# Performance work log

Measured on AMD Instinct MI355X. Metric: run time of the kernel, lower is better.

The kernel has to match this reference:

```python
import jax, jax.numpy as jnp
import numpy as np

B, N, D_IN, H = 4, 4096, 3072, 64
ADJ_DENSITY = 0.01


def _layernorm(x, g, b, eps=1e-5):
    mu = jnp.mean(x, axis=-1, keepdims=True)
    var = jnp.var(x, axis=-1, keepdims=True)
    return (x - mu) * jax.lax.rsqrt(var + eps) * g + b


def _gat(x, W, adj, concat):
    # x: [B, N, H], W: [H, H], adj: [N, N]
    Wh = jnp.matmul(x, W)                                   # [B, N, H]
    scores = jnp.einsum('bnh,bmh->bnm', Wh, Wh) / np.sqrt(H)  # [B, N, N]
    scores = jnp.where(adj > 0, scores, jnp.float32(-1e9))
    attn = jax.nn.softmax(scores, axis=2)                   # dropout: eval no-op
    h_prime = jnp.matmul(attn, Wh)                          # [B, N, H]
    return jax.nn.elu(h_prime) if concat else h_prime


def setup_inputs() -> dict:
    key = jax.random.key(0)
    ks = jax.random.split(key, 18)
    adj = (jax.random.uniform(ks[0], (N, N)) < ADJ_DENSITY).astype(jnp.float32)
    adj = jnp.maximum(adj, jnp.eye(N, dtype=jnp.float32))   # self loops

    def xavier(k, shape, gain=1.0):
        bound = gain * np.sqrt(6.0 / (shape[0] + shape[1]))
        return jax.random.uniform(k, shape, jnp.float32, -bound, bound)

    return {
        'stim_features': jax.random.normal(ks[1], (B, D_IN), jnp.float32),
        'adj': adj,
        'W_enc1': xavier(ks[2], (D_IN, 2 * H)),
        'b_enc1': jnp.zeros((2 * H,), jnp.float32),
        'ln_g': jnp.ones((2 * H,), jnp.float32),
        'ln_b': jnp.zeros((2 * H,), jnp.float32),
        'W_enc2': xavier(ks[3], (2 * H, H)),
        'b_enc2': jnp.zeros((H,), jnp.float32),
        'voxel_emb': jax.random.normal(ks[4], (N, H), jnp.float32) * 0.01,
        'W_gat1': xavier(ks[5], (H, H), gain=1.414),
        'W_gat2': xavier(ks[6], (H, H), gain=1.414),
        'skip1_W': xavier(ks[7], (H, H)),
        'skip1_b': jnp.zeros((H,), jnp.float32),
        'skip2_W': xavier(ks[8], (H, H)),
        'skip2_b': jnp.zeros((H,), jnp.float32),
        'ro_W': xavier(ks[9], (H, 1)),
        'ro_b': jnp.zeros((1,), jnp.float32),
    }


def reference(stim_features, adj, W_enc1, b_enc1, ln_g, ln_b, W_enc2, b_enc2,
              voxel_emb, W_gat1, W_gat2, skip1_W, skip1_b, skip2_W, skip2_b,
              ro_W, ro_b):
    # stim encoder: Linear -> LayerNorm -> GELU -> (Dropout eval) -> Linear
    g = stim_features @ W_enc1 + b_enc1                     # [B, 2H]
    g = _layernorm(g, ln_g, ln_b)
    g = jax.nn.gelu(g, approximate=False)
    g = g @ W_enc2 + b_enc2                                 # [B, H]

    x = g[:, None, :] + voxel_emb[None, :, :]               # [B, N, H]

    x_res = x
    x = _gat(x, W_gat1, adj, concat=True)
    x = x + (x_res @ skip1_W + skip1_b)

    x_res = x
    x = _gat(x, W_gat2, adj, concat=False)
    x = x + (x_res @ skip2_W + skip2_b)

    pred = (x @ ro_W + ro_b)[..., 0]                        # [B, N]
    return pred
```

## Files before the change

### kernel.cpp

```cpp
#include <hip/hip_runtime.h>
#include <math.h>

#define NB 4
#define NV 4096
#define DIN 3072
#define HD 64
#define CAP 80

typedef unsigned short u16;
typedef unsigned int u32;
typedef _Float16 h2 __attribute__((ext_vector_type(2)));

__device__ __forceinline__ float fdot2u(u32 v, u32 q, float c) {
#if __has_builtin(__builtin_amdgcn_fdot2)
  return __builtin_amdgcn_fdot2(__builtin_bit_cast(h2, v), __builtin_bit_cast(h2, q), c, false);
#else
  h2 a = __builtin_bit_cast(h2, v), b = __builtin_bit_cast(h2, q);
  return c + (float)a[0] * (float)b[0] + (float)a[1] * (float)b[1];
#endif
}

__device__ __forceinline__ h2 shx(h2 v, int off) {
  return __builtin_bit_cast(h2, (u32)__shfl_xor((int)__builtin_bit_cast(u32, v), off, 64));
}

__global__ __launch_bounds__(256) void pre_kernel(
    const float* __restrict__ adj, int* __restrict__ cnt, int* __restrict__ cols,
    const float* __restrict__ stim, const float* __restrict__ W1, float* __restrict__ part) {
  int bid = blockIdx.x;
  int t = threadIdx.x;
  if (bid < NV) {
    int row = bid;
    int l = t & 63, w = t >> 6;
    __shared__ int wtot[4];
    __shared__ int stot;
    const float4* p = (const float4*)(adj + (size_t)row * NV);
    float4 v0 = p[t], v1 = p[t + 256], v2 = p[t + 512], v3 = p[t + 768];
    int c = (v0.x > 0.f) + (v0.y > 0.f) + (v0.z > 0.f) + (v0.w > 0.f) +
            (v1.x > 0.f) + (v1.y > 0.f) + (v1.z > 0.f) + (v1.w > 0.f) +
            (v2.x > 0.f) + (v2.y > 0.f) + (v2.z > 0.f) + (v2.w > 0.f) +
            (v3.x > 0.f) + (v3.y > 0.f) + (v3.z > 0.f) + (v3.w > 0.f);
    int val = c;
#pragma unroll
    for (int off = 1; off < 64; off <<= 1) {
      int tmp = __shfl_up(val, off, 64);
      if (l >= off) val += tmp;
    }
    if (l == 63) wtot[w] = val;
    __syncthreads();
    int base = 0;
    for (int i = 0; i < w; ++i) base += wtot[i];
    if (t == 255) {
      int s = base + val;
      s = s > CAP ? CAP : s;
      cnt[row] = s;
      stot = s;
    }
    int o = base + (val - c);
    int* cr = cols + row * CAP;
#define EMIT(vv, jj) if ((vv) > 0.f) { if (o < CAP) cr[o] = (jj); ++o; }
    int j0 = t * 4, j1 = (t + 256) * 4, j2 = (t + 512) * 4, j3 = (t + 768) * 4;
    EMIT(v0.x, j0) EMIT(v0.y, j0 + 1) EMIT(v0.z, j0 + 2) EMIT(v0.w, j0 + 3)
    EMIT(v1.x, j1) EMIT(v1.y, j1 + 1) EMIT(v1.z, j1 + 2) EMIT(v1.w, j1 + 3)
    EMIT(v2.x, j2) EMIT(v2.y, j2 + 1) EMIT(v2.z, j2 + 2) EMIT(v2.w, j2 + 3)
    EMIT(v3.x, j3) EMIT(v3.y, j3 + 1) EMIT(v3.z, j3 + 2) EMIT(v3.w, j3 + 3)
#undef EMIT
    __syncthreads();
    if (t < CAP && t >= stot) cr[t] = 0;
  } else {
    int e = bid - NV;
    int c = e % 24;
    int b = e / 24;
    int j = t & 127, h = t >> 7;
    int k0 = c * 128 + h * 64;
    float acc = 0.f;
#pragma unroll 8
    for (int k = 0; k < 64; ++k)
      acc += stim[b * DIN + k0 + k] * W1[(size_t)(k0 + k) * 128 + j];
    part[((b * 24 + c) * 2 + h) * 128 + j] = acc;
  }
}

__global__ __launch_bounds__(256) void whsk1_kernel(
    const float* __restrict__ part, const float* __restrict__ b1,
    const float* __restrict__ lng, const float* __restrict__ lnb,
    const float* __restrict__ W2, const float* __restrict__ b2,
    const float* __restrict__ emb, const float* __restrict__ Wg,
    const float* __restrict__ Sw, const float* __restrict__ Sb,
    u16* __restrict__ Whh, float* __restrict__ Sk) {
  __shared__ float wgt[4096];
  __shared__ float swt[4096];
  __shared__ float xst[64 * 33];
  __shared__ float sbs[64];
  __shared__ float act[128];
  __shared__ float red[128];
  __shared__ __align__(16) float gs[64];
  __shared__ float s_mu, s_var;
  int tid = threadIdx.x;
  int base = blockIdx.x * 32;
  int b = base >> 12;

  for (int i = tid; i < 1024; i += 256) {
    ((float4*)wgt)[i] = ((const float4*)Wg)[i];
    ((float4*)swt)[i] = ((const float4*)Sw)[i];
  }
  if (tid < 64) sbs[tid] = Sb[tid];
  if (tid < 128) {
    float hv = 0.f;
    for (int c = 0; c < 48; ++c) hv += part[(b * 48 + c) * 128 + tid];
    hv += b1[tid];
    act[tid] = hv;
    red[tid] = hv;
  }
  __syncthreads();
  for (int s = 64; s > 0; s >>= 1) {
    if (tid < s) red[tid] += red[tid + s];
    __syncthreads();
  }
  if (tid == 0) s_mu = red[0] * (1.f / 128.f);
  __syncthreads();
  if (tid < 128) { float dv = act[tid] - s_mu; red[tid] = dv * dv; }
  __syncthreads();
  for (int s = 64; s > 0; s >>= 1) {
    if (tid < s) red[tid] += red[tid + s];
    __syncthreads();
  }
  if (tid == 0) s_var = red[0] * (1.f / 128.f);
  __syncthreads();
  if (tid < 128) {
    float y = (act[tid] - s_mu) * rsqrtf(s_var + 1e-5f) * lng[tid] + lnb[tid];
    act[tid] = 0.5f * y * (1.f + erff(y * 0.70710678118f));
  }
  __syncthreads();
  if (tid < 64) {
    float a2 = 0.f;
    for (int k = 0; k < 128; ++k) a2 += act[k] * W2[k * 64 + tid];
    gs[tid] = a2 + b2[tid];
  }
  __syncthreads();
  for (int i4 = tid; i4 < 512; i4 += 256) {
    int rr = i4 >> 4, k0 = (i4 & 15) * 4;
    int n = (base + rr) & (NV - 1);
    float4 gv = *(const float4*)(gs + k0);
    float4 ev = *(const float4*)(emb + (size_t)n * 64 + k0);
    xst[(k0 + 0) * 33 + rr] = gv.x + ev.x;
    xst[(k0 + 1) * 33 + rr] = gv.y + ev.y;
    xst[(k0 + 2) * 33 + rr] = gv.z + ev.z;
    xst[(k0 + 3) * 33 + rr] = gv.w + ev.w;
  }
  __syncthreads();
  int cg = tid & 15;
  int r0 = tid >> 4;
  float4 aw0 = make_float4(0, 0, 0, 0), as0 = make_float4(0, 0, 0, 0);
  float4 aw1 = make_float4(0, 0, 0, 0), as1 = make_float4(0, 0, 0, 0);
#pragma unroll 4
  for (int k = 0; k < 64; ++k) {
    float4 wv = *(const float4*)&wgt[k * 64 + 4 * cg];
    float4 sv = *(const float4*)&swt[k * 64 + 4 * cg];
    float x0 = xst[k * 33 + r0];
    float x1v = xst[k * 33 + r0 + 16];
    aw0.x = fmaf(x0, wv.x, aw0.x); aw0.y = fmaf(x0, wv.y, aw0.y);
    aw0.z = fmaf(x0, wv.z, aw0.z); aw0.w = fmaf(x0, wv.w, aw0.w);
    as0.x = fmaf(x0, sv.x, as0.x); as0.y = fmaf(x0, sv.y, as0.y);
    as0.z = fmaf(x0, sv.z, as0.z); as0.w = fmaf(x0, sv.w, as0.w);
    aw1.x = fmaf(x1v, wv.x, aw1.x); aw1.y = fmaf(x1v, wv.y, aw1.y);
    aw1.z = fmaf(x1v, wv.z, aw1.z); aw1.w = fmaf(x1v, wv.w, aw1.w);
    as1.x = fmaf(x1v, sv.x, as1.x); as1.y = fmaf(x1v, sv.y, as1.y);
    as1.z = fmaf(x1v, sv.z, as1.z); as1.w = fmaf(x1v, sv.w, as1.w);
  }
  float4 sb4 = *(const float4*)&sbs[4 * cg];
  int grow0 = base + r0, grow1 = base + r0 + 16;
  ushort4 h0, h1;
  h0.x = __builtin_bit_cast(u16, (_Float16)aw0.x);
  h0.y = __builtin_bit_cast(u16, (_Float16)aw0.y);
  h0.z = __builtin_bit_cast(u16, (_Float16)aw0.z);
  h0.w = __builtin_bit_cast(u16, (_Float16)aw0.w);
  h1.x = __builtin_bit_cast(u16, (_Float16)aw1.x);
  h1.y = __builtin_bit_cast(u16, (_Float16)aw1.y);
  h1.z = __builtin_bit_cast(u16, (_Float16)aw1.z);
  h1.w = __builtin_bit_cast(u16, (_Float16)aw1.w);
  *(ushort4*)(Whh + (size_t)grow0 * 64 + 4 * cg) = h0;
  *(ushort4*)(Whh + (size_t)grow1 * 64 + 4 * cg) = h1;
  *(float4*)(Sk + (size_t)grow0 * 64 + 4 * cg) =
      make_float4(as0.x + sb4.x, as0.y + sb4.y, as0.z + sb4.z, as0.w + sb4.w);
  *(float4*)(Sk + (size_t)grow1 * 64 + 4 * cg) =
      make_float4(as1.x + sb4.x, as1.y + sb4.y, as1.z + sb4.z, as1.w + sb4.w);
}

__global__ __launch_bounds__(512) void attn_l1_kernel(
    const u16* __restrict__ Whh, const float* __restrict__ Sk,
    const int* __restrict__ cnt, const int* __restrict__ cols,
    const float* __restrict__ Wg2, const float* __restrict__ Sw2, const float* __restrict__ Sb2,
    u16* __restrict__ Whh2, float* __restrict__ Sk2) {
  __shared__ float wgt[4096];
  __shared__ float swt[4096];
  __shared__ float sbs[64];
  __shared__ float xl[8][64];
  int tid = threadIdx.x;
  int lane = tid & 63;
  int w = tid >> 6;
  int bid = blockIdx.x;
  int x = bid & 7;
  int gidx = bid >> 3;
  int b = x >> 1;
  int rowhalf = x & 1;
  int n = __builtin_amdgcn_readfirstlane(rowhalf * 2048 + gidx * 8 + w);
  int wid = b * NV + n;
  const u16* whhbase = Whh + (size_t)b * (NV * HD);
  int nn = __builtin_amdgcn_readfirstlane(cnt[n]);
  const int* cl = cols + n * CAP;
  int q = lane & 3;
  int gq = lane >> 2;

  for (int i = tid; i < 1024; i += 512) {
    ((float4*)wgt)[i] = ((const float4*)Wg2)[i];
    ((float4*)swt)[i] = ((const float4*)Sw2)[i];
  }
  if (tid < 64) sbs[tid] = Sb2[tid];

  const uint4* qr = (const uint4*)(whhbase + (size_t)n * HD);
  uint4 QA = qr[q];
  uint4 QB = qr[q + 4];

  float s[5], p[5];
  uint4 SA0, SB0, SA1, SB1, SA2, SB2;
#define SCORE_BLOCK(jb, SAv, SBv)                                                                \
  {                                                                                              \
    int j = (jb) * 16 + gq;                                                                      \
    int m = cl[j];                                                                               \
    const uint4* vr = (const uint4*)(whhbase + (size_t)m * HD);                                  \
    SAv = vr[q];                                                                                 \
    SBv = vr[q + 4];                                                                             \
    float t = 0.f;                                                                               \
    t = fdot2u(SAv.x, QA.x, t);                                                                  \
    t = fdot2u(SAv.y, QA.y, t);                                                                  \
    t = fdot2u(SAv.z, QA.z, t);                                                                  \
    t = fdot2u(SAv.w, QA.w, t);                                                                  \
    t = fdot2u(SBv.x, QB.x, t);                                                                  \
    t = fdot2u(SBv.y, QB.y, t);                                                                  \
    t = fdot2u(SBv.z, QB.z, t);                                                                  \
    t = fdot2u(SBv.w, QB.w, t);                                                                  \
    t += __shfl_xor(t, 1, 64);                                                                   \
    t += __shfl_xor(t, 2, 64);                                                                   \
    s[jb] = (j < nn) ? t * 0.125f : -1e30f;                                                      \
  }
  SCORE_BLOCK(0, SA0, SB0)
  SCORE_BLOCK(1, SA1, SB1)
  SCORE_BLOCK(2, SA2, SB2)
  s[3] = -1e30f;
  s[4] = -1e30f;
  bool tail = (nn > 48);
  if (tail) {
    uint4 TA, TB;
    SCORE_BLOCK(3, TA, TB)
    SCORE_BLOCK(4, TA, TB)
  }
#undef SCORE_BLOCK

  float mx = fmaxf(fmaxf(fmaxf(s[0], s[1]), fmaxf(s[2], s[3])), s[4]);
  mx = fmaxf(mx, __shfl_xor(mx, 4, 64));
  mx = fmaxf(mx, __shfl_xor(mx, 8, 64));
  mx = fmaxf(mx, __shfl_xor(mx, 16, 64));
  mx = fmaxf(mx, __shfl_xor(mx, 32, 64));
  float sum = 0.f;
#pragma unroll
  for (int jb = 0; jb < 5; ++jb) {
    p[jb] = (jb * 16 + gq < nn) ? __expf(s[jb] - mx) : 0.f;
    sum += p[jb];
  }
  sum += __shfl_xor(sum, 4, 64);
  sum += __shfl_xor(sum, 8, 64);
  sum += __shfl_xor(sum, 16, 64);
  sum += __shfl_xor(sum, 32, 64);
  float inv = 1.f / sum;

  h2 aa[8];
#pragma unroll
  for (int k = 0; k < 8; ++k) aa[k] = h2{(_Float16)0, (_Float16)0};
#define PV_ACC(pp, Av, Bv)                                                                       \
  {                                                                                              \
    _Float16 pf = (_Float16)(pp);                                                                \
    h2 ph = {pf, pf};                                                                            \
    aa[0] += __builtin_bit_cast(h2, (Av).x) * ph;                                                \
    aa[1] += __builtin_bit_cast(h2, (Av).y) * ph;                                                \
    aa[2] += __builtin_bit_cast(h2, (Av).z) * ph;                                                \
    aa[3] += __builtin_bit_cast(h2, (Av).w) * ph;                                                \
    aa[4] += __builtin_bit_cast(h2, (Bv).x) * ph;                                                \
    aa[5] += __builtin_bit_cast(h2, (Bv).y) * ph;                                                \
    aa[6] += __builtin_bit_cast(h2, (Bv).z) * ph;                                                \
    aa[7] += __builtin_bit_cast(h2, (Bv).w) * ph;                                                \
  }
  PV_ACC(p[0], SA0, SB0)
  PV_ACC(p[1], SA1, SB1)
  PV_ACC(p[2], SA2, SB2)
  if (tail) {
    int m3 = cl[48 + gq];
    const uint4* vr3 = (const uint4*)(whhbase + (size_t)m3 * HD);
    uint4 A3 = vr3[q], B3 = vr3[q + 4];
    PV_ACC(p[3], A3, B3)
    if (nn > 64) {
      int m4 = cl[64 + gq];
      const uint4* vr4 = (const uint4*)(whhbase + (size_t)m4 * HD);
      uint4 A4 = vr4[q], B4 = vr4[q + 4];
      PV_ACC(p[4], A4, B4)
    }
  }
#undef PV_ACC

  bool g1 = (gq & 1) != 0;
  h2 bb[4];
#pragma unroll
  for (int i = 0; i < 4; ++i) {
    h2 k = g1 ? aa[i + 4] : aa[i];
    h2 u = g1 ? aa[i] : aa[i + 4];
    bb[i] = k + shx(u, 4);
  }
  bool g2 = (gq & 2) != 0;
  h2 cc[2];
#pragma unroll
  for (int i = 0; i < 2; ++i) {
    h2 k = g2 ? bb[i + 2] : bb[i];
    h2 u = g2 ? bb[i] : bb[i + 2];
    cc[i] = k + shx(u, 8);
  }
  bool g4 = (gq & 4) != 0;
  h2 dd;
  {
    h2 k = g4 ? cc[1] : cc[0];
    h2 u = g4 ? cc[0] : cc[1];
    dd = k + shx(u, 16);
  }
  dd = dd + shx(dd, 32);
  int a = 8 * q + 32 * (gq & 1) + 4 * ((gq >> 1) & 1) + 2 * ((gq >> 2) & 1);
  float f0 = (float)dd[0] * inv;
  float f1 = (float)dd[1] * inv;

  float2 sk2 = *(const float2*)(Sk + (size_t)wid * HD + a);
  float o0 = (f0 > 0.f ? f0 : (__expf(f0) - 1.f)) + sk2.x;
  float o1 = (f1 > 0.f ? f1 : (__expf(f1) - 1.f)) + sk2.y;
  if ((gq & 8) == 0) {
    xl[w][a] = o0;
    xl[w][a + 1] = o1;
  }
  __syncthreads();

  if (tid < 128) {
    int cg = tid & 15;
    int r = tid >> 4;
    float4 aw = make_float4(0, 0, 0, 0), as = make_float4(0, 0, 0, 0);
#pragma unroll 4
    for (int k = 0; k < 64; ++k) {
      float4 wv = *(const float4*)&wgt[k * 64 + 4 * cg];
      float4 sv = *(const float4*)&swt[k * 64 + 4 * cg];
      float xv = xl[r][k];
      aw.x = fmaf(xv, wv.x, aw.x); aw.y = fmaf(xv, wv.y, aw.y);
      aw.z = fmaf(xv, wv.z, aw.z); aw.w = fmaf(xv, wv.w, aw.w);
      as.x = fmaf(xv, sv.x, as.x); as.y = fmaf(xv, sv.y, as.y);
      as.z = fmaf(xv, sv.z, as.z); as.w = fmaf(xv, sv.w, as.w);
    }
    int n_r = rowhalf * 2048 + gidx * 8 + r;
    size_t wid_r = (size_t)(b * NV + n_r) * 64 + 4 * cg;
    float4 sb4 = *(const float4*)&sbs[4 * cg];
    ushort4 hh;
    hh.x = __builtin_bit_cast(u16, (_Float16)aw.x);
    hh.y = __builtin_bit_cast(u16, (_Float16)aw.y);
    hh.z = __builtin_bit_cast(u16, (_Float16)aw.z);
    hh.w = __builtin_bit_cast(u16, (_Float16)aw.w);
    *(ushort4*)(Whh2 + wid_r) = hh;
    *(float4*)(Sk2 + wid_r) =
        make_float4(as.x + sb4.x, as.y + sb4.y, as.z + sb4.z, as.w + sb4.w);
  }
}

__global__ __launch_bounds__(256) void attn_l2_kernel(
    const u16* __restrict__ Whh, const float* __restrict__ Sk,
    const int* __restrict__ cnt, const int* __restrict__ cols,
    const float* __restrict__ roW, const float* __restrict__ rob, float* __restrict__ out) {
  int tid = threadIdx.x;
  int lane = tid & 63;
  int w = tid >> 6;
  int bid = blockIdx.x;
  int x = bid & 7;
  int gidx = bid >> 3;
  int b = x >> 1;
  int n = __builtin_amdgcn_readfirstlane((x & 1) * 2048 + gidx * 4 + w);
  int wid = b * NV + n;
  const u16* whhbase = Whh + (size_t)b * (NV * HD);
  int nn = __builtin_amdgcn_readfirstlane(cnt[n]);
  const int* cl = cols + n * CAP;
  int q = lane & 3;
  int gq = lane >> 2;

  const uint4* qr = (const uint4*)(whhbase + (size_t)n * HD);
  uint4 QA = qr[q];
  uint4 QB = qr[q + 4];

  float s[5], p[5];
  uint4 SA0, SB0, SA1, SB1, SA2, SB2;
#define SCORE_BLOCK(jb, SAv, SBv)                                                                \
  {                                                                                              \
    int j = (jb) * 16 + gq;                                                                      \
    int m = cl[j];                                                                               \
    const uint4* vr = (const uint4*)(whhbase + (size_t)m * HD);                                  \
    SAv = vr[q];                                                                                 \
    SBv = vr[q + 4];                                                                             \
    float t = 0.f;                                                                               \
    t = fdot2u(SAv.x, QA.x, t);                                                                  \
    t = fdot2u(SAv.y, QA.y, t);                                                                  \
    t = fdot2u(SAv.z, QA.z, t);                                                                  \
    t = fdot2u(SAv.w, QA.w, t);                                                                  \
    t = fdot2u(SBv.x, QB.x, t);                                                                  \
    t = fdot2u(SBv.y, QB.y, t);                                                                  \
    t = fdot2u(SBv.z, QB.z, t);                                                                  \
    t = fdot2u(SBv.w, QB.w, t);                                                                  \
    t += __shfl_xor(t, 1, 64);                                                                   \
    t += __shfl_xor(t, 2, 64);                                                                   \
    s[jb] = (j < nn) ? t * 0.125f : -1e30f;                                                      \
  }
  SCORE_BLOCK(0, SA0, SB0)
  SCORE_BLOCK(1, SA1, SB1)
  SCORE_BLOCK(2, SA2, SB2)
  s[3] = -1e30f;
  s[4] = -1e30f;
  bool tail = (nn > 48);
  if (tail) {
    uint4 TA, TB;
    SCORE_BLOCK(3, TA, TB)
    SCORE_BLOCK(4, TA, TB)
  }
#undef SCORE_BLOCK

  float mx = fmaxf(fmaxf(fmaxf(s[0], s[1]), fmaxf(s[2], s[3])), s[4]);
  mx = fmaxf(mx, __shfl_xor(mx, 4, 64));
  mx = fmaxf(mx, __shfl_xor(mx, 8, 64));
  mx = fmaxf(mx, __shfl_xor(mx, 16, 64));
  mx = fmaxf(mx, __shfl_xor(mx, 32, 64));
  float sum = 0.f;
#pragma unroll
  for (int jb = 0; jb < 5; ++jb) {
    p[jb] = (jb * 16 + gq < nn) ? __expf(s[jb] - mx) : 0.f;
    sum += p[jb];
  }
  sum += __shfl_xor(sum, 4, 64);
  sum += __shfl_xor(sum, 8, 64);
  sum += __shfl_xor(sum, 16, 64);
  sum += __shfl_xor(sum, 32, 64);
  float inv = 1.f / sum;

  h2 aa[8];
#pragma unroll
  for (int k = 0; k < 8; ++k) aa[k] = h2{(_Float16)0, (_Float16)0};
#define PV_ACC(pp, Av, Bv)                                                                       \
  {                                                                                              \
    _Float16 pf = (_Float16)(pp);                                                                \
    h2 ph = {pf, pf};                                                                            \
    aa[0] += __builtin_bit_cast(h2, (Av).x) * ph;                                                \
    aa[1] += __builtin_bit_cast(h2, (Av).y) * ph;                                                \
    aa[2] += __builtin_bit_cast(h2, (Av).z) * ph;                                                \
    aa[3] += __builtin_bit_cast(h2, (Av).w) * ph;                                                \
    aa[4] += __builtin_bit_cast(h2, (Bv).x) * ph;                                                \
    aa[5] += __builtin_bit_cast(h2, (Bv).y) * ph;                                                \
    aa[6] += __builtin_bit_cast(h2, (Bv).z) * ph;                                                \
    aa[7] += __builtin_bit_cast(h2, (Bv).w) * ph;                                                \
  }
  PV_ACC(p[0], SA0, SB0)
  PV_ACC(p[1], SA1, SB1)
  PV_ACC(p[2], SA2, SB2)
  if (tail) {
    int m3 = cl[48 + gq];
    const uint4* vr3 = (const uint4*)(whhbase + (size_t)m3 * HD);
    uint4 A3 = vr3[q], B3 = vr3[q + 4];
    PV_ACC(p[3], A3, B3)
    if (nn > 64) {
      int m4 = cl[64 + gq];
      const uint4* vr4 = (const uint4*)(whhbase + (size_t)m4 * HD);
      uint4 A4 = vr4[q], B4 = vr4[q + 4];
      PV_ACC(p[4], A4, B4)
    }
  }
#undef PV_ACC

  bool g1 = (gq & 1) != 0;
  h2 bb[4];
#pragma unroll
  for (int i = 0; i < 4; ++i) {
    h2 k = g1 ? aa[i + 4] : aa[i];
    h2 u = g1 ? aa[i] : aa[i + 4];
    bb[i] = k + shx(u, 4);
  }
  bool g2 = (gq & 2) != 0;
  h2 cc[2];
#pragma unroll
  for (int i = 0; i < 2; ++i) {
    h2 k = g2 ? bb[i + 2] : bb[i];
    h2 u = g2 ? bb[i] : bb[i + 2];
    cc[i] = k + shx(u, 8);
  }
  bool g4 = (gq & 4) != 0;
  h2 dd;
  {
    h2 k = g4 ? cc[1] : cc[0];
    h2 u = g4 ? cc[0] : cc[1];
    dd = k + shx(u, 16);
  }
  dd = dd + shx(dd, 32);
  int a = 8 * q + 32 * (gq & 1) + 4 * ((gq >> 1) & 1) + 2 * ((gq >> 2) & 1);
  float f0 = (float)dd[0] * inv;
  float f1 = (float)dd[1] * inv;

  float2 sk2 = *(const float2*)(Sk + (size_t)wid * HD + a);
  float2 ro2 = *(const float2*)(roW + a);
  float wsp = (f0 + sk2.x) * ro2.x + (f1 + sk2.y) * ro2.y;
  wsp += __shfl_xor(wsp, 1, 64);
  wsp += __shfl_xor(wsp, 2, 64);
  wsp += __shfl_xor(wsp, 4, 64);
  wsp += __shfl_xor(wsp, 8, 64);
  wsp += __shfl_xor(wsp, 16, 64);
  if (lane == 0) out[wid] = wsp + rob[0];
}

extern "C" void kernel_launch(void* const* d_in, const int* in_sizes, int n_in,
                              void* d_out, int out_size, void* d_ws, size_t ws_size,
                              hipStream_t stream) {
  const float* stim = (const float*)d_in[0];
  const float* adj  = (const float*)d_in[1];
  const float* W1   = (const float*)d_in[2];
  const float* b1   = (const float*)d_in[3];
  const float* lng  = (const float*)d_in[4];
  const float* lnb  = (const float*)d_in[5];
  const float* W2   = (const float*)d_in[6];
  const float* b2   = (const float*)d_in[7];
  const float* emb  = (const float*)d_in[8];
  const float* Wg1  = (const float*)d_in[9];
  const float* Wg2  = (const float*)d_in[10];
  const float* s1w  = (const float*)d_in[11];
  const float* s1b  = (const float*)d_in[12];
  const float* s2w  = (const float*)d_in[13];
  const float* s2b  = (const float*)d_in[14];
  const float* roW  = (const float*)d_in[15];
  const float* rob  = (const float*)d_in[16];
  float* out = (float*)d_out;

  char* ws = (char*)d_ws;
  float* part = (float*)(ws + 4096);
  int*   cnt  = (int*)(ws + 131072);
  int*   cols = (int*)(ws + 147456);
  u16*   Whh2 = (u16*)(ws + 1572864);
  float* Sk   = (float*)(ws + 5767168);
  float* Sk2  = (float*)(ws + 9961472);
  u16*   Whh  = (u16*)(ws + 14155776);

  pre_kernel<<<dim3(NV + 96), dim3(256), 0, stream>>>(adj, cnt, cols, stim, W1, part);
  whsk1_kernel<<<dim3(NB * NV / 32), dim3(256), 0, stream>>>(part, b1, lng, lnb, W2, b2,
                                                             emb, Wg1, s1w, s1b, Whh, Sk);
  attn_l1_kernel<<<dim3(NB * NV / 8), dim3(512), 0, stream>>>(Whh, Sk, cnt, cols,
                                                              Wg2, s2w, s2b, Whh2, Sk2);
  attn_l2_kernel<<<dim3(NB * NV / 4), dim3(256), 0, stream>>>(Whh2, Sk2, cnt, cols,
                                                              roW, rob, out);
}
```

Baseline: 61.13 us.

## Overlap adjacency compaction with Wh/skip projection by regrouping kernels

The encoder partial GEMV moves into its own small kernel. Adjacency CSR compaction and the Wh/skip1 projection are merged into one launch, so the large adjacency scan runs alongside the projection blocks instead of before them. The softmax exp for the tail neighbor blocks now runs only when the row has more than 48 neighbors. The merged kernel uses a union shared-memory buffer sized for the projection path, which may lower occupancy for the adjacency blocks.

```diff
diff --git a/kernel.cpp b/kernel.cpp
--- a/kernel.cpp
+++ b/kernel.cpp
@@ -24,16 +24,37 @@
   return __builtin_bit_cast(h2, (u32)__shfl_xor((int)__builtin_bit_cast(u32, v), off, 64));
 }
 
-__global__ __launch_bounds__(256) void pre_kernel(
+__global__ __launch_bounds__(256) void enc_a_kernel(const float* __restrict__ stim,
+                                                    const float* __restrict__ W1,
+                                                    float* __restrict__ part) {
+  int c = blockIdx.x;
+  int b = blockIdx.y;
+  int t = threadIdx.x;
+  int j = t & 127, h = t >> 7;
+  int k0 = c * 128 + h * 64;
+  float acc = 0.f;
+#pragma unroll 8
+  for (int k = 0; k < 64; ++k)
+    acc += stim[b * DIN + k0 + k] * W1[(size_t)(k0 + k) * 128 + j];
+  part[((b * 24 + c) * 2 + h) * 128 + j] = acc;
+}
+
+__global__ __launch_bounds__(256) void mid_kernel(
     const float* __restrict__ adj, int* __restrict__ cnt, int* __restrict__ cols,
-    const float* __restrict__ stim, const float* __restrict__ W1, float* __restrict__ part) {
+    const float* __restrict__ part, const float* __restrict__ b1,
+    const float* __restrict__ lng, const float* __restrict__ lnb,
+    const float* __restrict__ W2, const float* __restrict__ b2,
+    const float* __restrict__ emb, const float* __restrict__ Wg,
+    const float* __restrict__ Sw, const float* __restrict__ Sb,
+    u16* __restrict__ Whh, float* __restrict__ Sk) {
+  __shared__ __align__(16) char smem[42784];
   int bid = blockIdx.x;
   int t = threadIdx.x;
   if (bid < NV) {
+    int* wtot = (int*)smem;
+    int* stot = (int*)(smem + 16);
     int row = bid;
     int l = t & 63, w = t >> 6;
-    __shared__ int wtot[4];
-    __shared__ int stot;
     const float4* p = (const float4*)(adj + (size_t)row * NV);
     float4 v0 = p[t], v1 = p[t + 256], v2 = p[t + 512], v3 = p[t + 768];
     int c = (v0.x > 0.f) + (v0.y > 0.f) + (v0.z > 0.f) + (v0.w > 0.f) +
@@ -54,7 +75,7 @@
       int s = base + val;
       s = s > CAP ? CAP : s;
       cnt[row] = s;
-      stot = s;
+      *stot = s;
     }
     int o = base + (val - c);
     int* cr = cols + row * CAP;
@@ -66,125 +87,107 @@
     EMIT(v3.x, j3) EMIT(v3.y, j3 + 1) EMIT(v3.z, j3 + 2) EMIT(v3.w, j3 + 3)
 #undef EMIT
     __syncthreads();
-    if (t < CAP && t >= stot) cr[t] = 0;
+    if (t < CAP && t >= *stot) cr[t] = 0;
   } else {
-    int e = bid - NV;
-    int c = e % 24;
-    int b = e / 24;
-    int j = t & 127, h = t >> 7;
-    int k0 = c * 128 + h * 64;
-    float acc = 0.f;
-#pragma unroll 8
-    for (int k = 0; k < 64; ++k)
-      acc += stim[b * DIN + k0 + k] * W1[(size_t)(k0 + k) * 128 + j];
-    part[((b * 24 + c) * 2 + h) * 128 + j] = acc;
-  }
-}
-
-__global__ __launch_bounds__(256) void whsk1_kernel(
-    const float* __restrict__ part, const float* __restrict__ b1,
-    const float* __restrict__ lng, const float* __restrict__ lnb,
-    const float* __restrict__ W2, const float* __restrict__ b2,
-    const float* __restrict__ emb, const float* __restrict__ Wg,
-    const float* __restrict__ Sw, const float* __restrict__ Sb,
-    u16* __restrict__ Whh, float* __restrict__ Sk) {
-  __shared__ float wgt[4096];
-  __shared__ float swt[4096];
-  __shared__ float xst[64 * 33];
-  __shared__ float sbs[64];
-  __shared__ float act[128];
-  __shared__ float red[128];
-  __shared__ __align__(16) float gs[64];
-  __shared__ float s_mu, s_var;
-  int tid = threadIdx.x;
-  int base = blockIdx.x * 32;
-  int b = base >> 12;
-
-  for (int i = tid; i < 1024; i += 256) {
-    ((float4*)wgt)[i] = ((const float4*)Wg)[i];
-    ((float4*)swt)[i] = ((const float4*)Sw)[i];
-  }
-  if (tid < 64) sbs[tid] = Sb[tid];
-  if (tid < 128) {
-    float hv = 0.f;
-    for (int c = 0; c < 48; ++c) hv += part[(b * 48 + c) * 128 + tid];
-    hv += b1[tid];
-    act[tid] = hv;
-    red[tid] = hv;
-  }
-  __syncthreads();
-  for (int s = 64; s > 0; s >>= 1) {
-    if (tid < s) red[tid] += red[tid + s];
-    __syncthreads();
-  }
-  if (tid == 0) s_mu = red[0] * (1.f / 128.f);
-  __syncthreads();
-  if (tid < 128) { float dv = act[tid] - s_mu; red[tid] = dv * dv; }
-  __syncthreads();
-  for (int s = 64; s > 0; s >>= 1) {
-    if (tid < s) red[tid] += red[tid + s];
-    __syncthreads();
-  }
-  if (tid == 0) s_var = red[0] * (1.f / 128.f);
-  __syncthreads();
-  if (tid < 128) {
-    float y = (act[tid] - s_mu) * rsqrtf(s_var + 1e-5f) * lng[tid] + lnb[tid];
-    act[tid] = 0.5f * y * (1.f + erff(y * 0.70710678118f));
-  }
-  __syncthreads();
-  if (tid < 64) {
-    float a2 = 0.f;
-    for (int k = 0; k < 128; ++k) a2 += act[k] * W2[k * 64 + tid];
-    gs[tid] = a2 + b2[tid];
-  }
-  __syncthreads();
-  for (int i4 = tid; i4 < 512; i4 += 256) {
-    int rr = i4 >> 4, k0 = (i4 & 15) * 4;
-    int n = (base + rr) & (NV - 1);
-    float4 gv = *(const float4*)(gs + k0);
-    float4 ev = *(const float4*)(emb + (size_t)n * 64 + k0);
-    xst[(k0 + 0) * 33 + rr] = gv.x + ev.x;
-    xst[(k0 + 1) * 33 + rr] = gv.y + ev.y;
-    xst[(k0 + 2) * 33 + rr] = gv.z + ev.z;
-    xst[(k0 + 3) * 33 + rr] = gv.w + ev.w;
-  }
-  __syncthreads();
-  int cg = tid & 15;
-  int r0 = tid >> 4;
-  float4 aw0 = make_float4(0, 0, 0, 0), as0 = make_float4(0, 0, 0, 0);
-  float4 aw1 = make_float4(0, 0, 0, 0), as1 = make_float4(0, 0, 0, 0);
+    float* wgt = (float*)smem;
+    float* swt = (float*)(smem + 16384);
+    float* xst = (float*)(smem + 32768);
+    float* sbs = (float*)(smem + 41216);
+    float* act = (float*)(smem + 41472);
+    float* red = (float*)(smem + 41984);
+    float* gs  = (float*)(smem + 42496);
+    float* s_mu = (float*)(smem + 42752);
+    float* s_var = (float*)(smem + 42756);
+    int tid = t;
+    int base = (bid - NV) * 32;
+    int b = base >> 12;
+
+    for (int i = tid; i < 1024; i += 256) {
+      ((float4*)wgt)[i] = ((const float4*)Wg)[i];
+      ((float4*)swt)[i] = ((const float4*)Sw)[i];
+    }
+    if (tid < 64) sbs[tid] = Sb[tid];
+    if (tid < 128) {
+      float hv = 0.f;
+      for (int c = 0; c < 48; ++c) hv += part[(b * 48 + c) * 128 + tid];
+      hv += b1[tid];
+      act[tid] = hv;
+      red[tid] = hv;
+    }
+    __syncthreads();
+    for (int s = 64; s > 0; s >>= 1) {
+      if (tid < s) red[tid] += red[tid + s];
+      __syncthreads();
+    }
+    if (tid == 0) *s_mu = red[0] * (1.f / 128.f);
+    __syncthreads();
+    if (tid < 128) { float dv = act[tid] - *s_mu; red[tid] = dv * dv; }
+    __syncthreads();
+    for (int s = 64; s > 0; s >>= 1) {
+      if (tid < s) red[tid] += red[tid + s];
+      __syncthreads();
+    }
+    if (tid == 0) *s_var = red[0] * (1.f / 128.f);
+    __syncthreads();
+    if (tid < 128) {
+      float y = (act[tid] - *s_mu) * rsqrtf(*s_var + 1e-5f) * lng[tid] + lnb[tid];
+      act[tid] = 0.5f * y * (1.f + erff(y * 0.70710678118f));
+    }
+    __syncthreads();
+    if (tid < 64) {
+      float a2 = 0.f;
+      for (int k = 0; k < 128; ++k) a2 += act[k] * W2[k * 64 + tid];
+      gs[tid] = a2 + b2[tid];
+    }
+    __syncthreads();
+    for (int i4 = tid; i4 < 512; i4 += 256) {
+      int rr = i4 >> 4, k0 = (i4 & 15) * 4;
+      int n = (base + rr) & (NV - 1);
+      float4 gv = *(const float4*)(gs + k0);
+      float4 ev = *(const float4*)(emb + (size_t)n * 64 + k0);
+      xst[(k0 + 0) * 33 + rr] = gv.x + ev.x;
+      xst[(k0 + 1) * 33 + rr] = gv.y + ev.y;
+      xst[(k0 + 2) * 33 + rr] = gv.z + ev.z;
+      xst[(k0 + 3) * 33 + rr] = gv.w + ev.w;
+    }
+    __syncthreads();
+    int cg = tid & 15;
+    int r0 = tid >> 4;
+    float4 aw0 = make_float4(0, 0, 0, 0), as0 = make_float4(0, 0, 0, 0);
+    float4 aw1 = make_float4(0, 0, 0, 0), as1 = make_float4(0, 0, 0, 0);
 #pragma unroll 4
-  for (int k = 0; k < 64; ++k) {
-    float4 wv = *(const float4*)&wgt[k * 64 + 4 * cg];
-    float4 sv = *(const float4*)&swt[k * 64 + 4 * cg];
-    float x0 = xst[k * 33 + r0];
-    float x1v = xst[k * 33 + r0 + 16];
-    aw0.x = fmaf(x0, wv.x, aw0.x); aw0.y = fmaf(x0, wv.y, aw0.y);
-    aw0.z = fmaf(x0, wv.z, aw0.z); aw0.w = fmaf(x0, wv.w, aw0.w);
-    as0.x = fmaf(x0, sv.x, as0.x); as0.y = fmaf(x0, sv.y, as0.y);
-    as0.z = fmaf(x0, sv.z, as0.z); as0.w = fmaf(x0, sv.w, as0.w);
-    aw1.x = fmaf(x1v, wv.x, aw1.x); aw1.y = fmaf(x1v, wv.y, aw1.y);
-    aw1.z = fmaf(x1v, wv.z, aw1.z); aw1.w = fmaf(x1v, wv.w, aw1.w);
-    as1.x = fmaf(x1v, sv.x, as1.x); as1.y = fmaf(x1v, sv.y, as1.y);
-    as1.z = fmaf(x1v, sv.z, as1.z); as1.w = fmaf(x1v, sv.w, as1.w);
-  }
-  float4 sb4 = *(const float4*)&sbs[4 * cg];
-  int grow0 = base + r0, grow1 = base + r0 + 16;
-  ushort4 h0, h1;
-  h0.x = __builtin_bit_cast(u16, (_Float16)aw0.x);
-  h0.y = __builtin_bit_cast(u16, (_Float16)aw0.y);
-  h0.z = __builtin_bit_cast(u16, (_Float16)aw0.z);
-  h0.w = __builtin_bit_cast(u16, (_Float16)aw0.w);
-  h1.x = __builtin_bit_cast(u16, (_Float16)aw1.x);
-  h1.y = __builtin_bit_cast(u16, (_Float16)aw1.y);
-  h1.z = __builtin_bit_cast(u16, (_Float16)aw1.z);
-  h1.w = __builtin_bit_cast(u16, (_Float16)aw1.w);
-  *(ushort4*)(Whh + (size_t)grow0 * 64 + 4 * cg) = h0;
-  *(ushort4*)(Whh + (size_t)grow1 * 64 + 4 * cg) = h1;
-  *(float4*)(Sk + (size_t)grow0 * 64 + 4 * cg) =
-      make_float4(as0.x + sb4.x, as0.y + sb4.y, as0.z + sb4.z, as0.w + sb4.w);
-  *(float4*)(Sk + (size_t)grow1 * 64 + 4 * cg) =
-      make_float4(as1.x + sb4.x, as1.y + sb4.y, as1.z + sb4.z, as1.w + sb4.w);
+    for (int k = 0; k < 64; ++k) {
+      float4 wv = *(const float4*)&wgt[k * 64 + 4 * cg];
+      float4 sv = *(const float4*)&swt[k * 64 + 4 * cg];
+      float x0 = xst[k * 33 + r0];
+      float x1v = xst[k * 33 + r0 + 16];
+      aw0.x = fmaf(x0, wv.x, aw0.x); aw0.y = fmaf(x0, wv.y, aw0.y);
+      aw0.z = fmaf(x0, wv.z, aw0.z); aw0.w = fmaf(x0, wv.w, aw0.w);
+      as0.x = fmaf(x0, sv.x, as0.x); as0.y = fmaf(x0, sv.y, as0.y);
+      as0.z = fmaf(x0, sv.z, as0.z); as0.w = fmaf(x0, sv.w, as0.w);
+      aw1.x = fmaf(x1v, wv.x, aw1.x); aw1.y = fmaf(x1v, wv.y, aw1.y);
+      aw1.z = fmaf(x1v, wv.z, aw1.z); aw1.w = fmaf(x1v, wv.w, aw1.w);
+      as1.x = fmaf(x1v, sv.x, as1.x); as1.y = fmaf(x1v, sv.y, as1.y);
+      as1.z = fmaf(x1v, sv.z, as1.z); as1.w = fmaf(x1v, sv.w, as1.w);
+    }
+    float4 sb4 = *(const float4*)&sbs[4 * cg];
+    int grow0 = base + r0, grow1 = base + r0 + 16;
+    ushort4 h0, h1;
+    h0.x = __builtin_bit_cast(u16, (_Float16)aw0.x);
+    h0.y = __builtin_bit_cast(u16, (_Float16)aw0.y);
+    h0.z = __builtin_bit_cast(u16, (_Float16)aw0.z);
+    h0.w = __builtin_bit_cast(u16, (_Float16)aw0.w);
+    h1.x = __builtin_bit_cast(u16, (_Float16)aw1.x);
+    h1.y = __builtin_bit_cast(u16, (_Float16)aw1.y);
+    h1.z = __builtin_bit_cast(u16, (_Float16)aw1.z);
+    h1.w = __builtin_bit_cast(u16, (_Float16)aw1.w);
+    *(ushort4*)(Whh + (size_t)grow0 * 64 + 4 * cg) = h0;
+    *(ushort4*)(Whh + (size_t)grow1 * 64 + 4 * cg) = h1;
+    *(float4*)(Sk + (size_t)grow0 * 64 + 4 * cg) =
+        make_float4(as0.x + sb4.x, as0.y + sb4.y, as0.z + sb4.z, as0.w + sb4.w);
+    *(float4*)(Sk + (size_t)grow1 * 64 + 4 * cg) =
+        make_float4(as1.x + sb4.x, as1.y + sb4.y, as1.z + sb4.z, as1.w + sb4.w);
+  }
 }
 
 __global__ __launch_bounds__(512) void attn_l1_kernel(
@@ -264,9 +267,16 @@
   mx = fmaxf(mx, __shfl_xor(mx, 32, 64));
   float sum = 0.f;
 #pragma unroll
-  for (int jb = 0; jb < 5; ++jb) {
+  for (int jb = 0; jb < 3; ++jb) {
     p[jb] = (jb * 16 + gq < nn) ? __expf(s[jb] - mx) : 0.f;
     sum += p[jb];
+  }
+  p[3] = 0.f;
+  p[4] = 0.f;
+  if (tail) {
+    p[3] = (48 + gq < nn) ? __expf(s[3] - mx) : 0.f;
+    p[4] = (64 + gq < nn) ? __expf(s[4] - mx) : 0.f;
+    sum += p[3] + p[4];
   }
   sum += __shfl_xor(sum, 4, 64);
   sum += __shfl_xor(sum, 8, 64);
@@ -437,9 +447,16 @@
   mx = fmaxf(mx, __shfl_xor(mx, 32, 64));
   float sum = 0.f;
 #pragma unroll
-  for (int jb = 0; jb < 5; ++jb) {
+  for (int jb = 0; jb < 3; ++jb) {
     p[jb] = (jb * 16 + gq < nn) ? __expf(s[jb] - mx) : 0.f;
     sum += p[jb];
+  }
+  p[3] = 0.f;
+  p[4] = 0.f;
+  if (tail) {
+    p[3] = (48 + gq < nn) ? __expf(s[3] - mx) : 0.f;
+    p[4] = (64 + gq < nn) ? __expf(s[4] - mx) : 0.f;
+    sum += p[3] + p[4];
   }
   sum += __shfl_xor(sum, 4, 64);
   sum += __shfl_xor(sum, 8, 64);
@@ -550,9 +567,9 @@
   float* Sk2  = (float*)(ws + 9961472);
   u16*   Whh  = (u16*)(ws + 14155776);
 
-  pre_kernel<<<dim3(NV + 96), dim3(256), 0, stream>>>(adj, cnt, cols, stim, W1, part);
-  whsk1_kernel<<<dim3(NB * NV / 32), dim3(256), 0, stream>>>(part, b1, lng, lnb, W2, b2,
-                                                             emb, Wg1, s1w, s1b, Whh, Sk);
+  enc_a_kernel<<<dim3(24, 4), dim3(256), 0, stream>>>(stim, W1, part);
+  mid_kernel<<<dim3(NV + 512), dim3(256), 0, stream>>>(adj, cnt, cols, part, b1, lng, lnb,
+                                                       W2, b2, emb, Wg1, s1w, s1b, Whh, Sk);
   attn_l1_kernel<<<dim3(NB * NV / 8), dim3(512), 0, stream>>>(Whh, Sk, cnt, cols,
                                                               Wg2, s2w, s2b, Whh2, Sk2);
   attn_l2_kernel<<<dim3(NB * NV / 4), dim3(256), 0, stream>>>(Whh2, Sk2, cnt, cols,
```

After: 64.80 us. 1.06x slower.
